# Optimization experiments

Measured on AMD Instinct MI355X. Metric: run time of the kernel, lower is better.

The kernel has to match this reference:

```python
import jax, jax.numpy as jnp
import numpy as np

B, H, SQ, SK, D = 2, 16, 2048, 2048, 128
P_DROP = 0.5


def setup_inputs() -> dict:
    key = jax.random.key(0)
    kq, kk, kv, km = jax.random.split(key, 4)
    query = jax.random.normal(kq, (B, H, SQ, D), dtype=jnp.float32)
    key_t = jax.random.normal(kk, (B, H, SK, D), dtype=jnp.float32)
    value = jax.random.normal(kv, (B, H, SK, D), dtype=jnp.float32)
    # deterministic Bernoulli(0.5) keep-mask standing in for dropout(p=0.5, train=True)
    dropout_mask = jax.random.randint(km, (B, H, SQ, SK), 0, 2, dtype=jnp.int32)
    return {"query": query, "key": key_t, "value": value, "dropout_mask": dropout_mask}


def reference(query, key, value, dropout_mask):
    d = query.shape[-1]
    # original: scaled_qk = qk.div(d ** -0.5)  ==  qk * sqrt(d)  (faithful to source)
    scale = jnp.asarray(d, query.dtype) ** 0.5
    qk = jnp.einsum("bhqd,bhkd->bhqk", query, key)  # [B,H,SQ,SK]
    scaled_qk = qk * scale
    keep_scale = jnp.asarray(1.0 / (1.0 - P_DROP), query.dtype)
    dropped = jnp.where(dropout_mask == 1, scaled_qk * keep_scale, jnp.zeros((), query.dtype))
    out = jnp.einsum("bhqk,bhkd->bhqd", dropped, value)  # [B,H,SQ,D]
    return out
```

## Files before the change

### kernel.cpp

```cpp
#include <hip/hip_runtime.h>
#include <hip/hip_bf16.h>

#define B_   2
#define H_   16
#define SQ_  2048
#define SK_  2048
#define D_   128
#define QT   128
#define KT   64
#define NITER (SK_/KT)

using bf16x8 = __attribute__((ext_vector_type(8))) __bf16;
using bf16x4 = __attribute__((ext_vector_type(4))) __bf16;
using f32x4  = __attribute__((ext_vector_type(4))) float;
using i32x4  = __attribute__((ext_vector_type(4))) int;

#define MFMA16(a,b,c) __builtin_amdgcn_mfma_f32_16x16x32_bf16(a,b,c,0,0,0)

#define QOFF 0u
#define KOFF (1u<<25)
#define VOFF (1u<<26)

#define KPITCH 136
#define VPITCH 72
#define PPITCH 72
#define KB_BYTES (KT*KPITCH*2)
#define VB_BYTES (D_*VPITCH*2)
#define PB_BYTES (QT*PPITCH*2)

__device__ __forceinline__ bf16x8 mask8(bf16x8 p, i32x4 a, i32x4 b) {
    bf16x8 r;
    r[0] = a[0] ? p[0] : (__bf16)0.0f;
    r[1] = a[1] ? p[1] : (__bf16)0.0f;
    r[2] = a[2] ? p[2] : (__bf16)0.0f;
    r[3] = a[3] ? p[3] : (__bf16)0.0f;
    r[4] = b[0] ? p[4] : (__bf16)0.0f;
    r[5] = b[1] ? p[5] : (__bf16)0.0f;
    r[6] = b[2] ? p[6] : (__bf16)0.0f;
    r[7] = b[3] ? p[7] : (__bf16)0.0f;
    return r;
}

__global__ __launch_bounds__(256)
void prep(const float* __restrict__ Q, const float* __restrict__ K,
          const float* __restrict__ V, char* __restrict__ ws)
{
    __shared__ __align__(16) __bf16 vlds[64 * 132];
    const int blk = blockIdx.x;
    const int t   = threadIdx.x;

    {
        const float4* q4 = (const float4*)Q;
        const float4* k4 = (const float4*)K;
        bf16x4* qd = (bf16x4*)(ws + QOFF);
        bf16x4* kd = (bf16x4*)(ws + KOFF);
        #pragma unroll
        for (int i = 0; i < 8; ++i) {
            size_t f = (size_t)blk * 2048 + t + 256 * i;
            float4 a = q4[f];
            qd[f] = (bf16x4){ (__bf16)a.x, (__bf16)a.y, (__bf16)a.z, (__bf16)a.w };
            float4 b = k4[f];
            kd[f] = (bf16x4){ (__bf16)b.x, (__bf16)b.y, (__bf16)b.z, (__bf16)b.w };
        }
    }
    {
        const float4* src = (const float4*)(V + (size_t)blk * KT * D_);
        #pragma unroll
        for (int i = 0; i < 8; ++i) {
            int f = t + 256 * i;
            float4 v = src[f];
            int row = f >> 5, col = f & 31;
            *(bf16x4*)&vlds[row * 132 + col * 4] =
                (bf16x4){ (__bf16)v.x, (__bf16)v.y, (__bf16)v.z, (__bf16)v.w };
        }
        __syncthreads();
        __bf16* dst = (__bf16*)(ws + VOFF) + (size_t)blk * (D_ * KT);
        const int d = t >> 1, h = t & 1;
        #pragma unroll
        for (int c = 0; c < 4; ++c) {
            bf16x8 frag;
            #pragma unroll
            for (int j = 0; j < 8; ++j) frag[j] = vlds[(h * 32 + c * 8 + j) * 132 + d];
            *(bf16x8*)&dst[d * KT + h * 32 + c * 8] = frag;
        }
    }
}

__global__ __launch_bounds__(256, 2)
void attn_drop_kernel(const char* __restrict__ ws,
                      const int*  __restrict__ M,
                      float* __restrict__ Out)
{
    __shared__ __align__(16) char smem[KB_BYTES + VB_BYTES + PB_BYTES];
    __bf16* Kb = (__bf16*)smem;
    __bf16* Vb = (__bf16*)(smem + KB_BYTES);
    __bf16* Pb = (__bf16*)(smem + KB_BYTES + VB_BYTES);

    const int tid  = threadIdx.x;
    const int wave = tid >> 6;
    const int lane = tid & 63;
    const int quad = lane >> 4;
    const int ln   = lane & 15;

    const int bh = blockIdx.x >> 4;
    const int qb = blockIdx.x & 15;

    const __bf16* Qbf = (const __bf16*)(ws + QOFF);
    const __bf16* Kbf = (const __bf16*)(ws + KOFF);
    const __bf16* Vtt = (const __bf16*)(ws + VOFF);
    const int* mbase = M + ((size_t)bh * SQ_ + (size_t)qb * QT) * SK_;
    float* optr = Out + ((size_t)bh * SQ_ + (size_t)qb * QT) * D_;

    bf16x8 qf[2][4];
    #pragma unroll
    for (int rt = 0; rt < 2; ++rt)
        #pragma unroll
        for (int s = 0; s < 4; ++s)
            qf[rt][s] = *(const bf16x8*)&Qbf[((size_t)bh*SQ_ + qb*QT + 32*wave + 16*rt + ln)*D_ + 32*s + 8*quad];

    f32x4 Oacc[2][8];
    #pragma unroll
    for (int rt = 0; rt < 2; ++rt)
        #pragma unroll
        for (int dt = 0; dt < 8; ++dt)
            Oacc[rt][dt] = (f32x4){0.f, 0.f, 0.f, 0.f};

    bf16x8 kreg[4], vreg[4];
    i32x4  mreg[2][2][2][2];
    {
        const __bf16* kp = Kbf + (size_t)bh * SK_ * D_;
        const __bf16* vp = Vtt + (size_t)(bh * 32) * (D_ * KT);
        #pragma unroll
        for (int j = 0; j < 4; ++j) {
            kreg[j] = *(const bf16x8*)&kp[j*2048 + tid*8];
            vreg[j] = *(const bf16x8*)&vp[j*2048 + tid*8];
        }
        #pragma unroll
        for (int rt = 0; rt < 2; ++rt)
            #pragma unroll
            for (int ks = 0; ks < 2; ++ks)
                #pragma unroll
                for (int i = 0; i < 2; ++i)
                    mreg[0][rt][ks][i] = __builtin_nontemporal_load(
                        (const i32x4*)&mbase[(size_t)(32*wave + 16*rt + ln)*SK_ + 32*ks + 8*quad + 4*i]);
    }

    #pragma unroll 2
    for (int kt = 0; kt < NITER; ++kt) {
        const int par = kt & 1;
        __syncthreads();
        #pragma unroll
        for (int j = 0; j < 4; ++j) {
            *(bf16x8*)&Kb[(16*j + (tid>>4))*KPITCH + (tid&15)*8] = kreg[j];
            *(bf16x8*)&Vb[(32*j + (tid>>3))*VPITCH + (tid&7)*8]  = vreg[j];
        }
        __syncthreads();

        {
            const int nkt = (kt + 1 < NITER) ? kt + 1 : kt;
            const __bf16* kp = Kbf + ((size_t)bh*SK_ + nkt*KT) * D_;
            const __bf16* vp = Vtt + (size_t)(bh*32 + nkt) * (D_*KT);
            #pragma unroll
            for (int j = 0; j < 4; ++j) {
                kreg[j] = *(const bf16x8*)&kp[j*2048 + tid*8];
                vreg[j] = *(const bf16x8*)&vp[j*2048 + tid*8];
            }
            #pragma unroll
            for (int rt = 0; rt < 2; ++rt)
                #pragma unroll
                for (int ks = 0; ks < 2; ++ks)
                    #pragma unroll
                    for (int i = 0; i < 2; ++i)
                        mreg[par^1][rt][ks][i] = __builtin_nontemporal_load(
                            (const i32x4*)&mbase[(size_t)(32*wave + 16*rt + ln)*SK_ + nkt*KT + 32*ks + 8*quad + 4*i]);
        }

        f32x4 S[2][4];
        #pragma unroll
        for (int rt = 0; rt < 2; ++rt)
            #pragma unroll
            for (int ct = 0; ct < 4; ++ct)
                S[rt][ct] = (f32x4){0.f, 0.f, 0.f, 0.f};

        #pragma unroll
        for (int s = 0; s < 4; ++s)
            #pragma unroll
            for (int ct = 0; ct < 4; ++ct) {
                bf16x8 kf = *(const bf16x8*)&Kb[(16*ct + ln)*KPITCH + 32*s + 8*quad];
                S[0][ct] = MFMA16(qf[0][s], kf, S[0][ct]);
                S[1][ct] = MFMA16(qf[1][s], kf, S[1][ct]);
            }

        #pragma unroll
        for (int rt = 0; rt < 2; ++rt)
            #pragma unroll
            for (int ct = 0; ct < 4; ++ct) {
                int row0 = 32*wave + 16*rt + 4*quad;
                #pragma unroll
                for (int r = 0; r < 4; ++r)
                    Pb[(row0 + r)*PPITCH + 16*ct + ln] = (__bf16)S[rt][ct][r];
            }

        #pragma unroll
        for (int ks = 0; ks < 2; ++ks) {
            bf16x8 pf0 = mask8(*(const bf16x8*)&Pb[(32*wave +      ln)*PPITCH + 32*ks + 8*quad],
                               mreg[par][0][ks][0], mreg[par][0][ks][1]);
            bf16x8 pf1 = mask8(*(const bf16x8*)&Pb[(32*wave + 16 + ln)*PPITCH + 32*ks + 8*quad],
                               mreg[par][1][ks][0], mreg[par][1][ks][1]);
            #pragma unroll
            for (int dt = 0; dt < 8; ++dt) {
                bf16x8 vf = *(const bf16x8*)&Vb[(16*dt + ln)*VPITCH + 32*ks + 8*quad];
                Oacc[0][dt] = MFMA16(pf0, vf, Oacc[0][dt]);
                Oacc[1][dt] = MFMA16(pf1, vf, Oacc[1][dt]);
            }
        }
    }

    const float SCALE = 22.62741699796952f;
    #pragma unroll
    for (int rt = 0; rt < 2; ++rt)
        #pragma unroll
        for (int dt = 0; dt < 8; ++dt) {
            int row0 = 32*wave + 16*rt + 4*quad;
            #pragma unroll
            for (int r = 0; r < 4; ++r)
                __builtin_nontemporal_store(Oacc[rt][dt][r] * SCALE,
                    &optr[(size_t)(row0 + r)*D_ + 16*dt + ln]);
        }
}

extern "C" void kernel_launch(void* const* d_in, const int* in_sizes, int n_in,
                              void* d_out, int out_size, void* d_ws, size_t ws_size,
                              hipStream_t stream) {
    (void)in_sizes; (void)n_in; (void)ws_size; (void)out_size;
    const float* Q = (const float*)d_in[0];
    const float* K = (const float*)d_in[1];
    const float* V = (const float*)d_in[2];
    const int*   M = (const int*)d_in[3];
    float* Out = (float*)d_out;
    char* ws = (char*)d_ws;

    prep<<<dim3(B_*H_*(SK_/KT)), 256, 0, stream>>>(Q, K, V, ws);
    attn_drop_kernel<<<dim3(B_*H_*(SQ_/QT)), 256, 0, stream>>>(ws, M, Out);
}
```

Before: 824.4 us.

## Precompress int32 dropout mask into bitmask in a separate kernel

Adds a pre-pass kernel that packs the int32 keep-mask into 64-bit bitmasks in workspace using wave shuffles. The attention kernel then loads one u64 per row per key tile instead of many int32 vectors, cutting register pressure and in-loop memory traffic, and the loop unroll is reduced to 1. The full mask must still be read once in the new pass, which can no longer overlap with the matrix compute and adds a launch.

```diff
diff --git a/kernel.cpp b/kernel.cpp
--- a/kernel.cpp
+++ b/kernel.cpp
@@ -9,17 +9,21 @@
 #define QT   128
 #define KT   64
 #define NITER (SK_/KT)
+#define MWORDS (SK_/64)
 
 using bf16x8 = __attribute__((ext_vector_type(8))) __bf16;
 using bf16x4 = __attribute__((ext_vector_type(4))) __bf16;
 using f32x4  = __attribute__((ext_vector_type(4))) float;
 using i32x4  = __attribute__((ext_vector_type(4))) int;
+typedef unsigned long long u64;
+typedef unsigned int u32;
 
 #define MFMA16(a,b,c) __builtin_amdgcn_mfma_f32_16x16x32_bf16(a,b,c,0,0,0)
 
 #define QOFF 0u
 #define KOFF (1u<<25)
 #define VOFF (1u<<26)
+#define MOFF (3u<<25)
 
 #define KPITCH 136
 #define VPITCH 72
@@ -28,17 +32,33 @@
 #define VB_BYTES (D_*VPITCH*2)
 #define PB_BYTES (QT*PPITCH*2)
 
-__device__ __forceinline__ bf16x8 mask8(bf16x8 p, i32x4 a, i32x4 b) {
+__device__ __forceinline__ bf16x8 mask8b(bf16x8 p, u32 byte) {
     bf16x8 r;
-    r[0] = a[0] ? p[0] : (__bf16)0.0f;
-    r[1] = a[1] ? p[1] : (__bf16)0.0f;
-    r[2] = a[2] ? p[2] : (__bf16)0.0f;
-    r[3] = a[3] ? p[3] : (__bf16)0.0f;
-    r[4] = b[0] ? p[4] : (__bf16)0.0f;
-    r[5] = b[1] ? p[5] : (__bf16)0.0f;
-    r[6] = b[2] ? p[6] : (__bf16)0.0f;
-    r[7] = b[3] ? p[7] : (__bf16)0.0f;
+    #pragma unroll
+    for (int e = 0; e < 8; ++e)
+        r[e] = (byte & (1u << e)) ? p[e] : (__bf16)0.0f;
     return r;
+}
+
+__global__ __launch_bounds__(256)
+void compress_mask(const int* __restrict__ M, char* __restrict__ ws)
+{
+    const int wave = threadIdx.x >> 6, lane = threadIdx.x & 63;
+    u64* out = (u64*)(ws + MOFF);
+    const int sh = 4 * (lane & 15);
+    #pragma unroll 2
+    for (int round = 0; round < 16; ++round) {
+        size_t base = (((size_t)blockIdx.x * 16 + round) * 4 + wave) * 256;
+        i32x4 m = __builtin_nontemporal_load((const i32x4*)(M + base) + lane);
+        u32 nib = (m[0] != 0) | ((m[1] != 0) << 1) | ((m[2] != 0) << 2) | ((m[3] != 0) << 3);
+        u64 v = (u64)nib << sh;
+        v |= __shfl_xor(v, 1);
+        v |= __shfl_xor(v, 2);
+        v |= __shfl_xor(v, 4);
+        v |= __shfl_xor(v, 8);
+        if ((lane & 15) == 0)
+            out[(base >> 6) + (lane >> 4)] = v;
+    }
 }
 
 __global__ __launch_bounds__(256)
@@ -48,7 +68,6 @@
     __shared__ __align__(16) __bf16 vlds[64 * 132];
     const int blk = blockIdx.x;
     const int t   = threadIdx.x;
-
     {
         const float4* q4 = (const float4*)Q;
         const float4* k4 = (const float4*)K;
@@ -87,9 +106,7 @@
 }
 
 __global__ __launch_bounds__(256, 2)
-void attn_drop_kernel(const char* __restrict__ ws,
-                      const int*  __restrict__ M,
-                      float* __restrict__ Out)
+void attn_drop_kernel(const char* __restrict__ ws, float* __restrict__ Out)
 {
     __shared__ __align__(16) char smem[KB_BYTES + VB_BYTES + PB_BYTES];
     __bf16* Kb = (__bf16*)smem;
@@ -101,6 +118,7 @@
     const int lane = tid & 63;
     const int quad = lane >> 4;
     const int ln   = lane & 15;
+    const int qs   = 8 * quad;
 
     const int bh = blockIdx.x >> 4;
     const int qb = blockIdx.x & 15;
@@ -108,8 +126,11 @@
     const __bf16* Qbf = (const __bf16*)(ws + QOFF);
     const __bf16* Kbf = (const __bf16*)(ws + KOFF);
     const __bf16* Vtt = (const __bf16*)(ws + VOFF);
-    const int* mbase = M + ((size_t)bh * SQ_ + (size_t)qb * QT) * SK_;
+    const u64*    Mb  = (const u64*)(ws + MOFF);
     float* optr = Out + ((size_t)bh * SQ_ + (size_t)qb * QT) * D_;
+
+    const size_t mrow0 = ((size_t)bh * SQ_ + qb * QT + 32 * wave + ln) * MWORDS;
+    const size_t mrow1 = mrow0 + 16 * MWORDS;
 
     bf16x8 qf[2][4];
     #pragma unroll
@@ -126,7 +147,7 @@
             Oacc[rt][dt] = (f32x4){0.f, 0.f, 0.f, 0.f};
 
     bf16x8 kreg[4], vreg[4];
-    i32x4  mreg[2][2][2][2];
+    u64 mcur0, mcur1;
     {
         const __bf16* kp = Kbf + (size_t)bh * SK_ * D_;
         const __bf16* vp = Vtt + (size_t)(bh * 32) * (D_ * KT);
@@ -135,19 +156,12 @@
             kreg[j] = *(const bf16x8*)&kp[j*2048 + tid*8];
             vreg[j] = *(const bf16x8*)&vp[j*2048 + tid*8];
         }
-        #pragma unroll
-        for (int rt = 0; rt < 2; ++rt)
-            #pragma unroll
-            for (int ks = 0; ks < 2; ++ks)
-                #pragma unroll
-                for (int i = 0; i < 2; ++i)
-                    mreg[0][rt][ks][i] = __builtin_nontemporal_load(
-                        (const i32x4*)&mbase[(size_t)(32*wave + 16*rt + ln)*SK_ + 32*ks + 8*quad + 4*i]);
-    }
-
-    #pragma unroll 2
+        mcur0 = Mb[mrow0];
+        mcur1 = Mb[mrow1];
+    }
+
+    #pragma unroll 1
     for (int kt = 0; kt < NITER; ++kt) {
-        const int par = kt & 1;
         __syncthreads();
         #pragma unroll
         for (int j = 0; j < 4; ++j) {
@@ -156,8 +170,9 @@
         }
         __syncthreads();
 
+        const int nkt = (kt + 1 < NITER) ? kt + 1 : kt;
+        u64 mnxt0, mnxt1;
         {
-            const int nkt = (kt + 1 < NITER) ? kt + 1 : kt;
             const __bf16* kp = Kbf + ((size_t)bh*SK_ + nkt*KT) * D_;
             const __bf16* vp = Vtt + (size_t)(bh*32 + nkt) * (D_*KT);
             #pragma unroll
@@ -165,14 +180,8 @@
                 kreg[j] = *(const bf16x8*)&kp[j*2048 + tid*8];
                 vreg[j] = *(const bf16x8*)&vp[j*2048 + tid*8];
             }
-            #pragma unroll
-            for (int rt = 0; rt < 2; ++rt)
-                #pragma unroll
-                for (int ks = 0; ks < 2; ++ks)
-                    #pragma unroll
-                    for (int i = 0; i < 2; ++i)
-                        mreg[par^1][rt][ks][i] = __builtin_nontemporal_load(
-                            (const i32x4*)&mbase[(size_t)(32*wave + 16*rt + ln)*SK_ + nkt*KT + 32*ks + 8*quad + 4*i]);
+            mnxt0 = Mb[mrow0 + nkt];
+            mnxt1 = Mb[mrow1 + nkt];
         }
 
         f32x4 S[2][4];
@@ -181,7 +190,6 @@
             #pragma unroll
             for (int ct = 0; ct < 4; ++ct)
                 S[rt][ct] = (f32x4){0.f, 0.f, 0.f, 0.f};
-
         #pragma unroll
         for (int s = 0; s < 4; ++s)
             #pragma unroll
@@ -203,10 +211,12 @@
 
         #pragma unroll
         for (int ks = 0; ks < 2; ++ks) {
-            bf16x8 pf0 = mask8(*(const bf16x8*)&Pb[(32*wave +      ln)*PPITCH + 32*ks + 8*quad],
-                               mreg[par][0][ks][0], mreg[par][0][ks][1]);
-            bf16x8 pf1 = mask8(*(const bf16x8*)&Pb[(32*wave + 16 + ln)*PPITCH + 32*ks + 8*quad],
-                               mreg[par][1][ks][0], mreg[par][1][ks][1]);
+            u32 h0 = (u32)(mcur0 >> (32 * ks));
+            u32 h1 = (u32)(mcur1 >> (32 * ks));
+            u32 b0 = (h0 >> qs) & 0xffu;
+            u32 b1 = (h1 >> qs) & 0xffu;
+            bf16x8 pf0 = mask8b(*(const bf16x8*)&Pb[(32*wave +      ln)*PPITCH + 32*ks + 8*quad], b0);
+            bf16x8 pf1 = mask8b(*(const bf16x8*)&Pb[(32*wave + 16 + ln)*PPITCH + 32*ks + 8*quad], b1);
             #pragma unroll
             for (int dt = 0; dt < 8; ++dt) {
                 bf16x8 vf = *(const bf16x8*)&Vb[(16*dt + ln)*VPITCH + 32*ks + 8*quad];
@@ -214,6 +224,8 @@
                 Oacc[1][dt] = MFMA16(pf1, vf, Oacc[1][dt]);
             }
         }
+        mcur0 = mnxt0;
+        mcur1 = mnxt1;
     }
 
     const float SCALE = 22.62741699796952f;
@@ -240,6 +252,7 @@
     float* Out = (float*)d_out;
     char* ws = (char*)d_ws;
 
+    compress_mask<<<dim3(8192), 256, 0, stream>>>(M, ws);
     prep<<<dim3(B_*H_*(SK_/KT)), 256, 0, stream>>>(Q, K, V, ws);
-    attn_drop_kernel<<<dim3(B_*H_*(SQ_/QT)), 256, 0, stream>>>(ws, M, Out);
-}
+    attn_drop_kernel<<<dim3(B_*H_*(SQ_/QT)), 256, 0, stream>>>(ws, Out);
+}
```

Measured after the change: 823.8 us. No clear change (-0.1%).
